# Optimization experiments

Measured on AMD Instinct MI355X. Metric: run time of the kernel, lower is better.

Reference implementation:

```python
import jax, jax.numpy as jnp
import numpy as np

D2 = 200  # 2*100 hardcoded in BiAttentionLayer.__init__
NEG = -10000000.0


def masked_softmax(v, m):
    # Faithful to the torch masked_softmax: softmax(v * m), re-mask, renormalize.
    r = jax.nn.softmax(v * m, axis=-1)
    r = r * m
    return r / (jnp.sum(r, axis=-1, keepdims=True) + 1e-13)


def setup_inputs() -> dict:
    key = jax.random.key(0)
    k0, k1, k2, k3, k4, k5 = jax.random.split(key, 6)
    N, T, J = 64, 1024, 64
    H = jax.random.normal(k0, (N, T, D2), jnp.float32)
    U = jax.random.normal(k1, (N, J, D2), jnp.float32)
    c_mask = jax.random.randint(k2, (N, T), 0, 2).astype(jnp.float32)
    q_mask = jax.random.randint(k3, (N, J), 0, 2).astype(jnp.float32)
    w = jax.random.normal(k4, (3 * D2,), jnp.float32) * 0.05  # Linear(3*d2, 1) weight
    b = jax.random.normal(k5, (), jnp.float32) * 0.05          # Linear bias
    return {"H": H, "U": U, "c_mask": c_mask, "q_mask": q_mask, "w": w, "b": b}


def reference(H, U, c_mask, q_mask, w, b):
    # Similarity: linear over concat(h, u, h*u) decomposed so the (N,T,J,3d)
    # intermediate is never materialized (same math as the torch module).
    w_h, w_u, w_hu = w[:D2], w[D2:2 * D2], w[2 * D2:]
    S = ((H @ w_h)[:, :, None]
         + (U @ w_u)[:, None, :]
         + jnp.einsum('ntd,njd->ntj', H * w_hu, U)
         + b)  # [N,T,J]

    # C2Q: masked softmax over question dim, attend over U.
    S_t = masked_softmax(S, q_mask[:, None, :])        # [N,T,J]
    U_ = jnp.einsum('ntj,njd->ntd', S_t, U)            # [N,T,d2]

    # Q2C: replace masked values with -1e7, max over J, softmax over context dim.
    qm = q_mask[:, None, :]
    S_rep = S * qm + NEG * (1.0 - qm)                  # [N,T,J]
    S_max = jnp.max(S_rep, axis=-1)                    # [N,T]
    a = masked_softmax(S_max, c_mask)                  # [N,T]
    H_ = jnp.einsum('nt,ntd->nd', a, H)[:, None, :]    # [N,1,d2] (broadcasts over T)

    G = jnp.concatenate([H, U_, H * U_, H * H_], axis=-1)  # [N,T,4*d2]
    return G
```

## Files before the change

kernel.cpp:

```cpp
#include <hip/hip_runtime.h>
#include <stdint.h>

#define NEGV -10000000.0f

typedef __attribute__((ext_vector_type(8))) short short8;
typedef __attribute__((ext_vector_type(4))) float f32x4;

__device__ __forceinline__ ushort f2b(float f) {
    uint32_t x = __float_as_uint(f);
    uint32_t r = x + 0x7FFFu + ((x >> 16) & 1u);
    return (ushort)(r >> 16);
}
__device__ __forceinline__ float b2f(ushort u) {
    union { float f; uint32_t i; } v; v.i = ((uint32_t)u) << 16; return v.f;
}

__launch_bounds__(256)
__global__ void k0_prep(const float* __restrict__ Ug, const float* __restrict__ wg,
                        const float* __restrict__ bg,
                        ushort* __restrict__ BhatW, ushort* __restrict__ UTW,
                        float* __restrict__ cW) {
    __shared__ __align__(16) float sU[64][204];
    __shared__ float sW[600];
    const int tid = threadIdx.x, lane = tid & 63, wid = tid >> 6;
    const int n = blockIdx.x;

    for (int i = tid; i < 600; i += 256) sW[i] = wg[i];
    for (int r = wid; r < 64; r += 4) {
        const float* urow = Ug + (size_t)(n * 64 + r) * 200;
        if (lane < 50) *(float4*)&sU[r][lane * 4] = *(const float4*)(urow + lane * 4);
    }
    __syncthreads();
    const float bval = bg[0];

    ushort* utn = UTW + (size_t)n * 224 * 64;
    for (int d = wid; d < 224; d += 4)
        utn[d * 64 + lane] = (d < 200) ? f2b(sU[lane][d]) : (ushort)0;

    ushort* bhn = BhatW + (size_t)n * 64 * 224;
    for (int r = wid; r < 64; r += 4) {
        float part = 0.f;
        for (int d = lane; d < 224; d += 64) {
            float bh = 0.f;
            if (d < 200) {
                float u = sU[r][d];
                bh = u * sW[400 + d] + sW[d];
                part += u * sW[200 + d];
            }
            bhn[r * 224 + d] = f2b(bh);
        }
        #pragma unroll
        for (int off = 32; off >= 1; off >>= 1) part += __shfl_xor(part, off);
        if (lane == 0) cW[n * 64 + r] = part + bval;
    }
}

__launch_bounds__(64)
__global__ void k13_fused(const float* __restrict__ Hg,
                          const ushort* __restrict__ BhatW,
                          const float* __restrict__ cW,
                          const float* __restrict__ qmg,
                          const ushort* __restrict__ UTW,
                          float* __restrict__ SmaxWs,
                          float* __restrict__ Gout) {
    __shared__ ushort sP[16][76];
    __shared__ ushort sU2[16][204];
    const int lane = threadIdx.x;
    const int g = lane >> 4, li = lane & 15;
    const int n = blockIdx.y, t0 = blockIdx.x * 16;

    const float*  Hrow = Hg + (size_t)(n * 1024 + t0 + li) * 200;
    const ushort* Bn   = BhatW + (size_t)n * 64 * 224;

    short8 av[7];
    #pragma unroll
    for (int kc = 0; kc < 7; ++kc) {
        if (kc < 6 || g == 0) {
            float4 h0 = *(const float4*)(Hrow + kc * 32 + g * 8);
            float4 h1 = *(const float4*)(Hrow + kc * 32 + g * 8 + 4);
            av[kc][0] = (short)f2b(h0.x); av[kc][1] = (short)f2b(h0.y);
            av[kc][2] = (short)f2b(h0.z); av[kc][3] = (short)f2b(h0.w);
            av[kc][4] = (short)f2b(h1.x); av[kc][5] = (short)f2b(h1.y);
            av[kc][6] = (short)f2b(h1.z); av[kc][7] = (short)f2b(h1.w);
        } else {
            av[kc] = (short8){0, 0, 0, 0, 0, 0, 0, 0};
        }
    }
    f32x4 acc[4];
    #pragma unroll
    for (int jt = 0; jt < 4; ++jt) acc[jt] = (f32x4){0.f, 0.f, 0.f, 0.f};
    #pragma unroll
    for (int kc = 0; kc < 7; ++kc) {
        #pragma unroll
        for (int jt = 0; jt < 4; ++jt) {
            short8 bv = *(const short8*)(Bn + (size_t)(jt * 16 + li) * 224 + kc * 32 + g * 8);
            acc[jt] = __builtin_amdgcn_mfma_f32_16x16x32_bf16(av[kc], bv, acc[jt], 0, 0, 0);
        }
    }

    float cj[4], qm[4];
    #pragma unroll
    for (int jt = 0; jt < 4; ++jt) {
        cj[jt] = cW[n * 64 + jt * 16 + li];
        qm[jt] = qmg[n * 64 + jt * 16 + li];
    }
    #pragma unroll
    for (int reg = 0; reg < 4; ++reg) {
        float x[4], y[4];
        float xm = -1e30f, ym = -1e30f;
        #pragma unroll
        for (int jt = 0; jt < 4; ++jt) {
            float s = acc[jt][reg] + cj[jt];
            x[jt] = s * qm[jt];
            y[jt] = (qm[jt] != 0.f) ? s : NEGV;
            xm = fmaxf(xm, x[jt]); ym = fmaxf(ym, y[jt]);
        }
        #pragma unroll
        for (int off = 1; off <= 8; off <<= 1) {
            xm = fmaxf(xm, __shfl_xor(xm, off));
            ym = fmaxf(ym, __shfl_xor(ym, off));
        }
        float e[4], z = 0.f, zm = 0.f;
        #pragma unroll
        for (int jt = 0; jt < 4; ++jt) {
            e[jt] = __expf(x[jt] - xm);
            z += e[jt]; zm += e[jt] * qm[jt];
        }
        #pragma unroll
        for (int off = 1; off <= 8; off <<= 1) {
            z  += __shfl_xor(z, off);
            zm += __shfl_xor(zm, off);
        }
        float inv = 1.f / (zm + 1e-13f * z);
        int trow = g * 4 + reg;
        #pragma unroll
        for (int jt = 0; jt < 4; ++jt) sP[trow][jt * 16 + li] = f2b(e[jt] * qm[jt] * inv);
        if (li == 0) SmaxWs[n * 1024 + t0 + trow] = ym;
    }

    const ushort* UTn = UTW + (size_t)n * 224 * 64;
    f32x4 acc2[13];
    #pragma unroll
    for (int dt = 0; dt < 13; ++dt) acc2[dt] = (f32x4){0.f, 0.f, 0.f, 0.f};
    #pragma unroll
    for (int kc = 0; kc < 2; ++kc) {
        short8 a2 = *(const short8*)(&sP[li][kc * 32 + g * 8]);
        #pragma unroll
        for (int dt = 0; dt < 13; ++dt) {
            short8 bv = *(const short8*)(UTn + (size_t)(dt * 16 + li) * 64 + kc * 32 + g * 8);
            acc2[dt] = __builtin_amdgcn_mfma_f32_16x16x32_bf16(a2, bv, acc2[dt], 0, 0, 0);
        }
    }

    #pragma unroll
    for (int dt = 0; dt < 13; ++dt) {
        int d = dt * 16 + li;
        if (d < 200) {
            #pragma unroll
            for (int reg = 0; reg < 4; ++reg)
                sU2[g * 4 + reg][d] = f2b(acc2[dt][reg]);
        }
    }

    for (int r = 0; r < 16; ++r) {
        if (lane < 50) {
            int d0 = lane * 4;
            const float* hrow = Hg + (size_t)(n * 1024 + t0 + r) * 200;
            float* orow = Gout + (size_t)(n * 1024 + t0 + r) * 800;
            f32x4 h = *(const f32x4*)(hrow + d0);
            uint2 uraw = *(const uint2*)&sU2[r][d0];
            f32x4 u;
            u[0] = b2f((ushort)(uraw.x & 0xffffu)); u[1] = b2f((ushort)(uraw.x >> 16));
            u[2] = b2f((ushort)(uraw.y & 0xffffu)); u[3] = b2f((ushort)(uraw.y >> 16));
            f32x4 hu = h * u;
            __builtin_nontemporal_store(h,  (f32x4*)(orow + d0));
            __builtin_nontemporal_store(u,  (f32x4*)(orow + 200 + d0));
            __builtin_nontemporal_store(hu, (f32x4*)(orow + 400 + d0));
        }
    }
}

__launch_bounds__(256)
__global__ void k2a_softmaxT(const float* __restrict__ cmg,
                             const float* __restrict__ SmaxWs,
                             float* __restrict__ aWs,
                             float* __restrict__ HbarWs) {
    __shared__ float red[8];
    const int tid = threadIdx.x, lane = tid & 63, wid = tid >> 6;
    const int n = blockIdx.x;

    float x[4], m[4];
    #pragma unroll
    for (int i = 0; i < 4; ++i) {
        int t = tid + 256 * i;
        float v = SmaxWs[n * 1024 + t];
        m[i] = cmg[(size_t)n * 1024 + t];
        x[i] = v * m[i];
    }
    float mx = fmaxf(fmaxf(x[0], x[1]), fmaxf(x[2], x[3]));
    #pragma unroll
    for (int off = 32; off >= 1; off >>= 1) mx = fmaxf(mx, __shfl_xor(mx, off));
    if (lane == 0) red[wid] = mx;
    __syncthreads();
    float M = fmaxf(fmaxf(red[0], red[1]), fmaxf(red[2], red[3]));
    __syncthreads();
    float e[4], z = 0.f, zm = 0.f;
    #pragma unroll
    for (int i = 0; i < 4; ++i) {
        e[i] = __expf(x[i] - M);
        z += e[i]; zm += e[i] * m[i];
    }
    #pragma unroll
    for (int off = 32; off >= 1; off >>= 1) {
        z  += __shfl_xor(z, off);
        zm += __shfl_xor(zm, off);
    }
    if (lane == 0) { red[wid] = z; red[4 + wid] = zm; }
    __syncthreads();
    float Z  = red[0] + red[1] + red[2] + red[3];
    float Zm = red[4] + red[5] + red[6] + red[7];
    float inv = 1.f / (Zm + 1e-13f * Z);
    #pragma unroll
    for (int i = 0; i < 4; ++i) aWs[n * 1024 + tid + 256 * i] = e[i] * m[i] * inv;
    if (tid < 200) HbarWs[n * 200 + tid] = 0.f;
}

__launch_bounds__(256)
__global__ void k2b_hbar(const float* __restrict__ Hg,
                         const float* __restrict__ aWs,
                         float* __restrict__ HbarWs) {
    __shared__ float sA[64];
    const int tid = threadIdx.x;
    const int n = blockIdx.y, t0 = blockIdx.x * 64;
    if (tid < 64) sA[tid] = aWs[n * 1024 + t0 + tid];
    __syncthreads();
    if (tid < 200) {
        const float* hp = Hg + (size_t)(n * 1024 + t0) * 200 + tid;
        float acc = 0.f;
        #pragma unroll 8
        for (int t = 0; t < 64; ++t) acc += sA[t] * hp[(size_t)t * 200];
        atomicAdd(HbarWs + n * 200 + tid, acc);
    }
}

__launch_bounds__(256)
__global__ void k4_hh(const float* __restrict__ Hg,
                      const float* __restrict__ HbarWs,
                      float* __restrict__ Gout) {
    __shared__ __align__(16) float sHb[200];
    const int tid = threadIdx.x, lane = tid & 63, wid = tid >> 6;
    const int n = blockIdx.y, t0 = blockIdx.x * 64;
    if (tid < 200) sHb[tid] = HbarWs[n * 200 + tid];
    __syncthreads();
    for (int r = wid; r < 64; r += 4) {
        if (lane < 50) {
            int d0 = lane * 4;
            const float* hrow = Hg + (size_t)(n * 1024 + t0 + r) * 200;
            float* orow = Gout + (size_t)(n * 1024 + t0 + r) * 800;
            f32x4 h  = *(const f32x4*)(hrow + d0);
            f32x4 hb = *(const f32x4*)&sHb[d0];
            f32x4 hh = h * hb;
            __builtin_nontemporal_store(hh, (f32x4*)(orow + 600 + d0));
        }
    }
}

extern "C" void kernel_launch(void* const* d_in, const int* in_sizes, int n_in,
                              void* d_out, int out_size, void* d_ws, size_t ws_size,
                              hipStream_t stream) {
    (void)in_sizes; (void)n_in; (void)out_size; (void)ws_size;
    const float* Hg  = (const float*)d_in[0];
    const float* Ug  = (const float*)d_in[1];
    const float* cmg = (const float*)d_in[2];
    const float* qmg = (const float*)d_in[3];
    const float* wg  = (const float*)d_in[4];
    const float* bg  = (const float*)d_in[5];
    float* Gout = (float*)d_out;

    char* ws = (char*)d_ws;
    float*  SmaxWs = (float*) (ws);
    float*  aWs    = (float*) (ws + 262144);
    float*  HbarWs = (float*) (ws + 524288);
    float*  cWs    = (float*) (ws + 575488);
    ushort* BhatWs = (ushort*)(ws + 591872);
    ushort* UTWs   = (ushort*)(ws + 2426880);

    dim3 blk256(256, 1, 1);
    k0_prep<<<dim3(64, 1, 1), blk256, 0, stream>>>(Ug, wg, bg, BhatWs, UTWs, cWs);
    k13_fused<<<dim3(64, 64, 1), dim3(64, 1, 1), 0, stream>>>(Hg, BhatWs, cWs, qmg,
                                                              UTWs, SmaxWs, Gout);
    k2a_softmaxT<<<dim3(64, 1, 1), blk256, 0, stream>>>(cmg, SmaxWs, aWs, HbarWs);
    k2b_hbar<<<dim3(16, 64, 1), blk256, 0, stream>>>(Hg, aWs, HbarWs);
    k4_hh<<<dim3(16, 64, 1), blk256, 0, stream>>>(Hg, HbarWs, Gout);
}
```

Before: 325.9 us.

## Prepack MFMA operand fragments, stage H in LDS, store G directly from accumulators

The prep kernel now writes both B operands (Bhat and U transposed) in per-lane MFMA fragment order, so each lane in the fused kernel loads one contiguous short8. The fused kernel loads its 16-row H tile once, coalesced, into LDS as bf16. That tile feeds the first GEMM and also the epilogue, which removes the second global read of H. The epilogue writes the H, U_ and H*U_ columns straight from the accumulator registers with scalar nontemporal stores instead of bouncing through LDS and writing float4s. The trade-offs are narrower, less vectorized output stores on a write-bound kernel, and H output columns that are now rounded to bf16 rather than copied exactly.

```diff
diff --git a/kernel.cpp b/kernel.cpp
--- a/kernel.cpp
+++ b/kernel.cpp
@@ -18,7 +18,7 @@
 __launch_bounds__(256)
 __global__ void k0_prep(const float* __restrict__ Ug, const float* __restrict__ wg,
                         const float* __restrict__ bg,
-                        ushort* __restrict__ BhatW, ushort* __restrict__ UTW,
+                        ushort* __restrict__ Bf, ushort* __restrict__ Uf,
                         float* __restrict__ cW) {
     __shared__ __align__(16) float sU[64][204];
     __shared__ float sW[600];
@@ -33,68 +33,93 @@
     __syncthreads();
     const float bval = bg[0];
 
-    ushort* utn = UTW + (size_t)n * 224 * 64;
-    for (int d = wid; d < 224; d += 4)
-        utn[d * 64 + lane] = (d < 200) ? f2b(sU[lane][d]) : (ushort)0;
-
-    ushort* bhn = BhatW + (size_t)n * 64 * 224;
+    ushort* bfn = Bf + (size_t)n * (28 * 512);
+    for (int item = tid; item < 28 * 64; item += 256) {
+        int chunk = item >> 6, l2 = item & 63;
+        int kc = chunk >> 2, jt = chunk & 3;
+        int g2 = l2 >> 4, li2 = l2 & 15;
+        int j = jt * 16 + li2;
+        int d0 = kc * 32 + g2 * 8;
+        short8 v;
+        #pragma unroll
+        for (int e = 0; e < 8; ++e) {
+            int d = d0 + e;
+            float bh = 0.f;
+            if (d < 200) bh = sU[j][d] * sW[400 + d] + sW[d];
+            v[e] = (short)f2b(bh);
+        }
+        *(short8*)(bfn + (size_t)item * 8) = v;
+    }
+
+    ushort* ufn = Uf + (size_t)n * (26 * 512);
+    for (int item = tid; item < 26 * 64; item += 256) {
+        int chunk = item >> 6, l2 = item & 63;
+        int kc2 = chunk / 13, dt = chunk % 13;
+        int g2 = l2 >> 4, li2 = l2 & 15;
+        int d = dt * 16 + li2;
+        int j0 = kc2 * 32 + g2 * 8;
+        short8 v;
+        #pragma unroll
+        for (int e = 0; e < 8; ++e)
+            v[e] = (d < 200) ? (short)f2b(sU[j0 + e][d]) : (short)0;
+        *(short8*)(ufn + (size_t)item * 8) = v;
+    }
+
     for (int r = wid; r < 64; r += 4) {
         float part = 0.f;
-        for (int d = lane; d < 224; d += 64) {
-            float bh = 0.f;
-            if (d < 200) {
-                float u = sU[r][d];
-                bh = u * sW[400 + d] + sW[d];
-                part += u * sW[200 + d];
-            }
-            bhn[r * 224 + d] = f2b(bh);
-        }
+        for (int d = lane; d < 200; d += 64) part += sU[r][d] * sW[200 + d];
         #pragma unroll
         for (int off = 32; off >= 1; off >>= 1) part += __shfl_xor(part, off);
         if (lane == 0) cW[n * 64 + r] = part + bval;
     }
 }
 
-__launch_bounds__(64)
+__launch_bounds__(64, 4)
 __global__ void k13_fused(const float* __restrict__ Hg,
-                          const ushort* __restrict__ BhatW,
+                          const ushort* __restrict__ Bf,
                           const float* __restrict__ cW,
                           const float* __restrict__ qmg,
-                          const ushort* __restrict__ UTW,
+                          const ushort* __restrict__ Uf,
                           float* __restrict__ SmaxWs,
                           float* __restrict__ Gout) {
-    __shared__ ushort sP[16][76];
-    __shared__ ushort sU2[16][204];
+    __shared__ __align__(16) ushort sHb[16][232];
+    __shared__ __align__(16) ushort sP[16][80];
     const int lane = threadIdx.x;
     const int g = lane >> 4, li = lane & 15;
     const int n = blockIdx.y, t0 = blockIdx.x * 16;
 
-    const float*  Hrow = Hg + (size_t)(n * 1024 + t0 + li) * 200;
-    const ushort* Bn   = BhatW + (size_t)n * 64 * 224;
-
-    short8 av[7];
+    const float* Hbase = Hg + (size_t)(n * 1024 + t0) * 200;
+    #pragma unroll
+    for (int it = 0; it < 13; ++it) {
+        int idx = lane + it * 64;
+        if (idx < 800) {
+            int row = idx / 50, c4 = (idx - row * 50) * 4;
+            float4 h = *(const float4*)(Hbase + (size_t)row * 200 + c4);
+            uint2 wv;
+            wv.x = ((uint)f2b(h.y) << 16) | (uint)f2b(h.x);
+            wv.y = ((uint)f2b(h.w) << 16) | (uint)f2b(h.z);
+            *(uint2*)&sHb[row][c4] = wv;
+        }
+    }
+    #pragma unroll
+    for (int it = 0; it < 4; ++it) {
+        int id2 = lane + it * 64;
+        int row = id2 >> 4, c = id2 & 15;
+        *(uint*)&sHb[row][200 + c * 2] = 0u;
+    }
+
+    const ushort* Bn = Bf + (size_t)n * (28 * 512);
+    f32x4 acc[4];
+    #pragma unroll
+    for (int jt = 0; jt < 4; ++jt) acc[jt] = (f32x4){0.f, 0.f, 0.f, 0.f};
+    const ushort* aRow = &sHb[li][g * 8];
     #pragma unroll
     for (int kc = 0; kc < 7; ++kc) {
-        if (kc < 6 || g == 0) {
-            float4 h0 = *(const float4*)(Hrow + kc * 32 + g * 8);
-            float4 h1 = *(const float4*)(Hrow + kc * 32 + g * 8 + 4);
-            av[kc][0] = (short)f2b(h0.x); av[kc][1] = (short)f2b(h0.y);
-            av[kc][2] = (short)f2b(h0.z); av[kc][3] = (short)f2b(h0.w);
-            av[kc][4] = (short)f2b(h1.x); av[kc][5] = (short)f2b(h1.y);
-            av[kc][6] = (short)f2b(h1.z); av[kc][7] = (short)f2b(h1.w);
-        } else {
-            av[kc] = (short8){0, 0, 0, 0, 0, 0, 0, 0};
-        }
-    }
-    f32x4 acc[4];
-    #pragma unroll
-    for (int jt = 0; jt < 4; ++jt) acc[jt] = (f32x4){0.f, 0.f, 0.f, 0.f};
-    #pragma unroll
-    for (int kc = 0; kc < 7; ++kc) {
+        short8 av = *(const short8*)(aRow + kc * 32);
         #pragma unroll
         for (int jt = 0; jt < 4; ++jt) {
-            short8 bv = *(const short8*)(Bn + (size_t)(jt * 16 + li) * 224 + kc * 32 + g * 8);
-            acc[jt] = __builtin_amdgcn_mfma_f32_16x16x32_bf16(av[kc], bv, acc[jt], 0, 0, 0);
+            short8 bv = *(const short8*)(Bn + (size_t)((kc * 4 + jt) * 64 + lane) * 8);
+            acc[jt] = __builtin_amdgcn_mfma_f32_16x16x32_bf16(av, bv, acc[jt], 0, 0, 0);
         }
     }
 
@@ -138,16 +163,16 @@
         if (li == 0) SmaxWs[n * 1024 + t0 + trow] = ym;
     }
 
-    const ushort* UTn = UTW + (size_t)n * 224 * 64;
+    const ushort* Un = Uf + (size_t)n * (26 * 512);
     f32x4 acc2[13];
     #pragma unroll
     for (int dt = 0; dt < 13; ++dt) acc2[dt] = (f32x4){0.f, 0.f, 0.f, 0.f};
     #pragma unroll
-    for (int kc = 0; kc < 2; ++kc) {
-        short8 a2 = *(const short8*)(&sP[li][kc * 32 + g * 8]);
+    for (int kc2 = 0; kc2 < 2; ++kc2) {
+        short8 a2 = *(const short8*)(&sP[li][kc2 * 32 + g * 8]);
         #pragma unroll
         for (int dt = 0; dt < 13; ++dt) {
-            short8 bv = *(const short8*)(UTn + (size_t)(dt * 16 + li) * 64 + kc * 32 + g * 8);
+            short8 bv = *(const short8*)(Un + (size_t)((kc2 * 13 + dt) * 64 + lane) * 8);
             acc2[dt] = __builtin_amdgcn_mfma_f32_16x16x32_bf16(a2, bv, acc2[dt], 0, 0, 0);
         }
     }
@@ -157,25 +182,15 @@
         int d = dt * 16 + li;
         if (d < 200) {
             #pragma unroll
-            for (int reg = 0; reg < 4; ++reg)
-                sU2[g * 4 + reg][d] = f2b(acc2[dt][reg]);
-        }
-    }
-
-    for (int r = 0; r < 16; ++r) {
-        if (lane < 50) {
-            int d0 = lane * 4;
-            const float* hrow = Hg + (size_t)(n * 1024 + t0 + r) * 200;
-            float* orow = Gout + (size_t)(n * 1024 + t0 + r) * 800;
-            f32x4 h = *(const f32x4*)(hrow + d0);
-            uint2 uraw = *(const uint2*)&sU2[r][d0];
-            f32x4 u;
-            u[0] = b2f((ushort)(uraw.x & 0xffffu)); u[1] = b2f((ushort)(uraw.x >> 16));
-            u[2] = b2f((ushort)(uraw.y & 0xffffu)); u[3] = b2f((ushort)(uraw.y >> 16));
-            f32x4 hu = h * u;
-            __builtin_nontemporal_store(h,  (f32x4*)(orow + d0));
-            __builtin_nontemporal_store(u,  (f32x4*)(orow + 200 + d0));
-            __builtin_nontemporal_store(hu, (f32x4*)(orow + 400 + d0));
+            for (int reg = 0; reg < 4; ++reg) {
+                int r = g * 4 + reg;
+                float h = b2f(sHb[r][d]);
+                float u = acc2[dt][reg];
+                float* orow = Gout + (size_t)(n * 1024 + t0 + r) * 800;
+                __builtin_nontemporal_store(h,     orow + d);
+                __builtin_nontemporal_store(u,     orow + 200 + d);
+                __builtin_nontemporal_store(h * u, orow + 400 + d);
+            }
         }
     }
 }
@@ -282,13 +297,13 @@
     float*  aWs    = (float*) (ws + 262144);
     float*  HbarWs = (float*) (ws + 524288);
     float*  cWs    = (float*) (ws + 575488);
-    ushort* BhatWs = (ushort*)(ws + 591872);
-    ushort* UTWs   = (ushort*)(ws + 2426880);
+    ushort* BfWs   = (ushort*)(ws + 591872);
+    ushort* UfWs   = (ushort*)(ws + 2426880);
 
     dim3 blk256(256, 1, 1);
-    k0_prep<<<dim3(64, 1, 1), blk256, 0, stream>>>(Ug, wg, bg, BhatWs, UTWs, cWs);
-    k13_fused<<<dim3(64, 64, 1), dim3(64, 1, 1), 0, stream>>>(Hg, BhatWs, cWs, qmg,
-                                                              UTWs, SmaxWs, Gout);
+    k0_prep<<<dim3(64, 1, 1), blk256, 0, stream>>>(Ug, wg, bg, BfWs, UfWs, cWs);
+    k13_fused<<<dim3(64, 64, 1), dim3(64, 1, 1), 0, stream>>>(Hg, BfWs, cWs, qmg,
+                                                              UfWs, SmaxWs, Gout);
     k2a_softmaxT<<<dim3(64, 1, 1), blk256, 0, stream>>>(cmg, SmaxWs, aWs, HbarWs);
     k2b_hbar<<<dim3(16, 64, 1), blk256, 0, stream>>>(Hg, aWs, HbarWs);
     k4_hh<<<dim3(16, 64, 1), blk256, 0, stream>>>(Hg, HbarWs, Gout);
```

After: 372.6 us. 14.3% more time.
